# Performance work log

Measured on AMD Instinct MI355X. Metric: run time of the kernel, lower is better.

The kernel has to match this reference:

```python
import jax, jax.numpy as jnp
import numpy as np

H_GRID, W_GRID = 32, 32
KH, KW = 7, 11
NUM_HEADS = 8


def local_window_mask(H, W, kh, kw):
    # Token (h,w) may attend to (h',w') iff |h-h'|<=kh//2 and |w-w'|<=kw//2
    # (equivalent to the padded/cropped construction in the torch module).
    hh = jnp.arange(H)
    ww = jnp.arange(W)
    ok_h = jnp.abs(hh[:, None] - hh[None, :]) <= kh // 2  # [H,H]
    ok_w = jnp.abs(ww[:, None] - ww[None, :]) <= kw // 2  # [W,W]
    ok = ok_h[:, None, :, None] & ok_w[None, :, None, :]  # [H,W,H,W]
    ok = ok.reshape(H * W, H * W)
    return jnp.where(ok, 0.0, -jnp.inf)[None, None]  # [1,1,N,N]


def setup_inputs() -> dict:
    key = jax.random.key(0)
    k1, k2, k3, k4, k5 = jax.random.split(key, 5)
    B, N, E = 8, H_GRID * W_GRID, 256
    return {
        "x": jax.random.normal(k1, (B, N, E), dtype=jnp.float32),
        "qkv_w": jax.random.normal(k2, (3 * E, E), dtype=jnp.float32) * 0.02,
        "qkv_b": jax.random.normal(k3, (3 * E,), dtype=jnp.float32) * 0.02,
        "proj_w": jax.random.normal(k4, (E, E), dtype=jnp.float32) * 0.02,
        "proj_b": jax.random.normal(k5, (E,), dtype=jnp.float32) * 0.02,
    }


def reference(x, qkv_w, qkv_b, proj_w, proj_b):
    B, N, E = x.shape
    dh = E // NUM_HEADS
    scale = E ** (-0.5)  # note: embed_dim scaling, as in the original module
    qkv = x @ qkv_w.T + qkv_b                       # [B,N,3E]
    qkv = qkv.reshape(B, N, 3, NUM_HEADS, dh).transpose(2, 0, 3, 1, 4)
    q, k, v = qkv[0] * scale, qkv[1], qkv[2]        # [B,H,N,dh]
    attn = jnp.einsum('bhnd,bhmd->bhnm', q, k)      # [B,H,N,N]
    attn = attn + local_window_mask(H_GRID, W_GRID, KH, KW)
    attn = jax.nn.softmax(attn, axis=-1)
    out = jnp.einsum('bhnm,bhmd->bhnd', attn, v)    # [B,H,N,dh]
    out = out.transpose(0, 2, 1, 3).reshape(B, N, E)
    return out @ proj_w.T + proj_b
```

## Files before the change

### kernel.cpp

```cpp
#include <hip/hip_runtime.h>
#include <math.h>

constexpr int Bb = 8;
constexpr int Ns = 1024;
constexpr int Es = 256;
constexpr int NH = 8;
constexpr int DH = 32;
constexpr int Mrows = Bb * Ns;
constexpr int NX = Mrows * Es;
constexpr int NQ = 3 * Es * Es;
constexpr int NP = Es * Es;

typedef __bf16 bf16x8 __attribute__((ext_vector_type(8)));
typedef float  f32x4  __attribute__((ext_vector_type(4)));
union U4B8 { uint4 u; bf16x8 b; unsigned short s[8]; };

__device__ __forceinline__ unsigned short f2bf(float f) {
    union { float f; unsigned u; } c; c.f = f;
    unsigned r = (c.u + 0x7FFFu + ((c.u >> 16) & 1u)) >> 16;
    return (unsigned short)r;
}
__device__ __forceinline__ float bf2f(unsigned short h) {
    union { unsigned u; float f; } c; c.u = ((unsigned)h) << 16;
    return c.f;
}

#define GLD 72
#define PST 232

__global__ __launch_bounds__(256)
void cast_all(const float* __restrict__ x, const float* __restrict__ wq,
              const float* __restrict__ wp, unsigned short* __restrict__ xb,
              unsigned short* __restrict__ wqb, unsigned short* __restrict__ wpb)
{
    int i = (blockIdx.x * 256 + threadIdx.x) * 8;
    const float* src; unsigned short* dst;
    if (i < NX)            { src = x  + i;             dst = xb  + i; }
    else if (i < NX + NQ)  { src = wq + (i - NX);      dst = wqb + (i - NX); }
    else                   { src = wp + (i - NX - NQ); dst = wpb + (i - NX - NQ); }
    float4 f0 = *(const float4*)src;
    float4 f1 = *(const float4*)(src + 4);
    U4B8 u;
    u.s[0] = f2bf(f0.x); u.s[1] = f2bf(f0.y); u.s[2] = f2bf(f0.z); u.s[3] = f2bf(f0.w);
    u.s[4] = f2bf(f1.x); u.s[5] = f2bf(f1.y); u.s[6] = f2bf(f1.z); u.s[7] = f2bf(f1.w);
    *(uint4*)dst = u.u;
}

__global__ __launch_bounds__(256, 4)
void qkv_gemm(const unsigned short* __restrict__ A, const unsigned short* __restrict__ W,
              const float* __restrict__ qkv_b,
              unsigned short* __restrict__ qo, unsigned short* __restrict__ ko,
              unsigned short* __restrict__ vto)
{
    __shared__ unsigned short As[64 * GLD];
    __shared__ unsigned short Ws[64 * GLD];

    const int t = threadIdx.x;
    const int m0 = (blockIdx.x & 127) * 64;
    const int j0 = (blockIdx.x >> 7) * 64;

    const int srow = t >> 2;
    const int scol = (t & 3) * 16;

    const int lane = t & 63;
    const int wave = t >> 6;
    const int wm = (wave & 1) * 32;
    const int wn = (wave >> 1) * 32;
    const int fm = lane & 15;
    const int fq = lane >> 4;

    f32x4 acc[2][2];
    #pragma unroll
    for (int i = 0; i < 2; i++)
        #pragma unroll
        for (int j = 0; j < 2; j++)
            acc[i][j] = (f32x4){0.f, 0.f, 0.f, 0.f};

    const unsigned short* Arow = A + (size_t)(m0 + srow) * Es;
    const unsigned short* Wrow = W + (size_t)(j0 + srow) * Es;

    for (int k0 = 0; k0 < Es; k0 += 64) {
        uint4 a0 = *(const uint4*)(Arow + k0 + scol);
        uint4 a1 = *(const uint4*)(Arow + k0 + scol + 8);
        uint4 w0 = *(const uint4*)(Wrow + k0 + scol);
        uint4 w1 = *(const uint4*)(Wrow + k0 + scol + 8);
        __syncthreads();
        *(uint4*)&As[srow * GLD + scol]     = a0;
        *(uint4*)&As[srow * GLD + scol + 8] = a1;
        *(uint4*)&Ws[srow * GLD + scol]     = w0;
        *(uint4*)&Ws[srow * GLD + scol + 8] = w1;
        __syncthreads();
        #pragma unroll
        for (int ks = 0; ks < 64; ks += 32) {
            U4B8 af0, af1, bf0, bf1;
            af0.u = *(const uint4*)&As[(wm +      fm) * GLD + ks + fq * 8];
            af1.u = *(const uint4*)&As[(wm + 16 + fm) * GLD + ks + fq * 8];
            bf0.u = *(const uint4*)&Ws[(wn +      fm) * GLD + ks + fq * 8];
            bf1.u = *(const uint4*)&Ws[(wn + 16 + fm) * GLD + ks + fq * 8];
            acc[0][0] = __builtin_amdgcn_mfma_f32_16x16x32_bf16(af0.b, bf0.b, acc[0][0], 0, 0, 0);
            acc[0][1] = __builtin_amdgcn_mfma_f32_16x16x32_bf16(af0.b, bf1.b, acc[0][1], 0, 0, 0);
            acc[1][0] = __builtin_amdgcn_mfma_f32_16x16x32_bf16(af1.b, bf0.b, acc[1][0], 0, 0, 0);
            acc[1][1] = __builtin_amdgcn_mfma_f32_16x16x32_bf16(af1.b, bf1.b, acc[1][1], 0, 0, 0);
        }
    }

    #pragma unroll
    for (int mt = 0; mt < 2; mt++) {
        #pragma unroll
        for (int nt = 0; nt < 2; nt++) {
            #pragma unroll
            for (int r = 0; r < 4; r++) {
                int row = m0 + wm + mt * 16 + fq * 4 + r;
                int col = j0 + wn + nt * 16 + fm;
                float val = acc[mt][nt][r] + qkv_b[col];
                int part = col >> 8;
                int head = (col >> 5) & 7;
                int d = col & 31;
                int b = row >> 10;
                int n = row & 1023;
                int bh = b * NH + head;
                if (part == 0)
                    qo[((size_t)bh * Ns + n) * DH + d] = f2bf(val * 0.0625f);
                else if (part == 1)
                    ko[((size_t)bh * Ns + n) * DH + d] = f2bf(val);
                else
                    vto[((size_t)bh * DH + d) * Ns + n] = f2bf(val);
            }
        }
    }
}

__global__ __launch_bounds__(256)
void attn_mfma2(const unsigned short* __restrict__ qb, const unsigned short* __restrict__ kb,
                const unsigned short* __restrict__ vtb, unsigned short* __restrict__ aob)
{
    __shared__ unsigned short Pb[32 * PST];
    __shared__ float psum[2][32];

    const int blk = blockIdx.x;
    const int b   = blk & 7;
    const int u   = blk >> 3;
    const int h   = u & 7;
    const int hq  = u >> 3;
    const int bh  = b * NH + h;

    const int t   = threadIdx.x;
    const int lane = t & 63;
    const int w    = t >> 6;
    const int fm = lane & 15;
    const int fq = lane >> 4;

    int n0c = (hq - 3) * 32;
    n0c = n0c < 0 ? 0 : (n0c > Ns - 224 ? Ns - 224 : n0c);

    const int qbase = (w & 1) * 16;
    const int sel   = w >> 1;
    const int dbase = (w >> 1) * 16;

    const unsigned short* vrow = vtb + ((size_t)bh * DH + dbase + fm) * Ns;
    uint4 vpre[7];
    #pragma unroll
    for (int i = 0; i < 7; i++)
        vpre[i] = *(const uint4*)(vrow + n0c + i * 32 + fq * 8);

    U4B8 qa;
    qa.u = *(const uint4*)(qb + ((size_t)bh * Ns + hq * 32 + qbase + fm) * DH + fq * 8);

    f32x4 sv[7];
    #pragma unroll
    for (int i = 0; i < 7; i++) {
        int kt = sel + 2 * i;
        U4B8 kf;
        kf.u = *(const uint4*)(kb + ((size_t)bh * Ns + n0c + kt * 16 + fm) * DH + fq * 8);
        sv[i] = __builtin_amdgcn_mfma_f32_16x16x32_bf16(qa.b, kf.b, (f32x4){0.f,0.f,0.f,0.f}, 0, 0, 0);
    }

    float sm[4] = {0.f, 0.f, 0.f, 0.f};
    #pragma unroll
    for (int i = 0; i < 7; i++) {
        int kt = sel + 2 * i;
        int g = n0c + kt * 16 + fm;
        int gh = g >> 5, gw = g & 31;
        int dhh = gh - hq;
        bool okh = (dhh >= -3) && (dhh <= 3);
        #pragma unroll
        for (int r = 0; r < 4; r++) {
            int qc = qbase + fq * 4 + r;
            int dww = gw - qc;
            bool ok = okh && (dww >= -5) && (dww <= 5);
            float p = ok ? __expf(sv[i][r]) : 0.f;
            unsigned short pu = f2bf(p);
            Pb[qc * PST + kt * 16 + fm] = pu;
            sm[r] += bf2f(pu);
        }
    }
    #pragma unroll
    for (int r = 0; r < 4; r++)
        #pragma unroll
        for (int m = 1; m < 16; m <<= 1)
            sm[r] += __shfl_xor(sm[r], m);
    if (fm == 0) {
        #pragma unroll
        for (int r = 0; r < 4; r++)
            psum[sel][qbase + fq * 4 + r] = sm[r];
    }
    __syncthreads();

    f32x4 acc = (f32x4){0.f, 0.f, 0.f, 0.f};
    #pragma unroll
    for (int i = 0; i < 7; i++) {
        U4B8 pa, vb;
        pa.u = *(const uint4*)&Pb[(qbase + fm) * PST + i * 32 + fq * 8];
        vb.u = vpre[i];
        acc = __builtin_amdgcn_mfma_f32_16x16x32_bf16(pa.b, vb.b, acc, 0, 0, 0);
    }

    #pragma unroll
    for (int r = 0; r < 4; r++) {
        int qq = qbase + fq * 4 + r;
        float inv = 1.f / (psum[0][qq] + psum[1][qq]);
        aob[((size_t)(b * Ns) + hq * 32 + qq) * Es + h * DH + dbase + fm] = f2bf(acc[r] * inv);
    }
}

__global__ __launch_bounds__(256, 4)
void proj_gemm(const unsigned short* __restrict__ A, const unsigned short* __restrict__ Wb,
               const float* __restrict__ bias, float* __restrict__ out)
{
    __shared__ unsigned short As[64 * GLD];
    __shared__ unsigned short Ws[64 * GLD];

    const int t = threadIdx.x;
    const int m0 = (blockIdx.x & 127) * 64;
    const int j0 = (blockIdx.x >> 7) * 64;

    const int srow = t >> 2;
    const int scol = (t & 3) * 16;

    const int lane = t & 63;
    const int wave = t >> 6;
    const int wm = (wave & 1) * 32;
    const int wn = (wave >> 1) * 32;
    const int fm = lane & 15;
    const int fq = lane >> 4;

    f32x4 acc[2][2];
    #pragma unroll
    for (int i = 0; i < 2; i++)
        #pragma unroll
        for (int j = 0; j < 2; j++)
            acc[i][j] = (f32x4){0.f, 0.f, 0.f, 0.f};

    const unsigned short* Arow = A + (size_t)(m0 + srow) * Es;
    const unsigned short* Wrow = Wb + (size_t)(j0 + srow) * Es;

    for (int k0 = 0; k0 < Es; k0 += 64) {
        uint4 a0 = *(const uint4*)(Arow + k0 + scol);
        uint4 a1 = *(const uint4*)(Arow + k0 + scol + 8);
        uint4 w0 = *(const uint4*)(Wrow + k0 + scol);
        uint4 w1 = *(const uint4*)(Wrow + k0 + scol + 8);
        __syncthreads();
        *(uint4*)&As[srow * GLD + scol]     = a0;
        *(uint4*)&As[srow * GLD + scol + 8] = a1;
        *(uint4*)&Ws[srow * GLD + scol]     = w0;
        *(uint4*)&Ws[srow * GLD + scol + 8] = w1;
        __syncthreads();
        #pragma unroll
        for (int ks = 0; ks < 64; ks += 32) {
            U4B8 af0, af1, bf0, bf1;
            af0.u = *(const uint4*)&As[(wm +      fm) * GLD + ks + fq * 8];
            af1.u = *(const uint4*)&As[(wm + 16 + fm) * GLD + ks + fq * 8];
            bf0.u = *(const uint4*)&Ws[(wn +      fm) * GLD + ks + fq * 8];
            bf1.u = *(const uint4*)&Ws[(wn + 16 + fm) * GLD + ks + fq * 8];
            acc[0][0] = __builtin_amdgcn_mfma_f32_16x16x32_bf16(af0.b, bf0.b, acc[0][0], 0, 0, 0);
            acc[0][1] = __builtin_amdgcn_mfma_f32_16x16x32_bf16(af0.b, bf1.b, acc[0][1], 0, 0, 0);
            acc[1][0] = __builtin_amdgcn_mfma_f32_16x16x32_bf16(af1.b, bf0.b, acc[1][0], 0, 0, 0);
            acc[1][1] = __builtin_amdgcn_mfma_f32_16x16x32_bf16(af1.b, bf1.b, acc[1][1], 0, 0, 0);
        }
    }

    #pragma unroll
    for (int mt = 0; mt < 2; mt++) {
        #pragma unroll
        for (int nt = 0; nt < 2; nt++) {
            #pragma unroll
            for (int r = 0; r < 4; r++) {
                int row = m0 + wm + mt * 16 + fq * 4 + r;
                int col = j0 + wn + nt * 16 + fm;
                out[(size_t)row * Es + col] = acc[mt][nt][r] + bias[col];
            }
        }
    }
}

extern "C" void kernel_launch(void* const* d_in, const int* in_sizes, int n_in,
                              void* d_out, int out_size, void* d_ws, size_t ws_size,
                              hipStream_t stream) {
    const float* x      = (const float*)d_in[0];
    const float* qkv_w  = (const float*)d_in[1];
    const float* qkv_b  = (const float*)d_in[2];
    const float* proj_w = (const float*)d_in[3];
    const float* proj_b = (const float*)d_in[4];
    float* out = (float*)d_out;

    unsigned short* xb  = (unsigned short*)d_ws;
    unsigned short* wqb = xb + NX;
    unsigned short* pwb = wqb + NQ;
    unsigned short* qb  = pwb + NP;
    unsigned short* kb  = qb + NX;
    unsigned short* vtb = kb + NX;
    unsigned short* aob = vtb + NX;

    cast_all<<<dim3((NX + NQ + NP) / 8 / 256), dim3(256), 0, stream>>>(
        x, qkv_w, proj_w, xb, wqb, pwb);

    qkv_gemm<<<dim3(1536), dim3(256), 0, stream>>>(xb, wqb, qkv_b, qb, kb, vtb);

    attn_mfma2<<<dim3(Bb * NH * 32), dim3(256), 0, stream>>>(qb, kb, vtb, aob);

    proj_gemm<<<dim3(128 * 4), dim3(256), 0, stream>>>(aob, pwb, proj_b, out);
}
```

Measured before the change: 101.2 us.

## Fuse all four stages into one persistent kernel with grid barriers

```diff
diff --git a/kernel.cpp b/kernel.cpp
--- a/kernel.cpp
+++ b/kernel.cpp
@@ -11,6 +11,13 @@
 constexpr int NQ = 3 * Es * Es;
 constexpr int NP = Es * Es;
 
+constexpr int CAST_UNITS = (NX + NQ + NP) / (8 * 256);
+constexpr int QKV_TILES  = 1536;
+constexpr int ATTN_TILES = Bb * NH * 32;
+constexpr int PROJ_TILES = 512;
+
+constexpr int GRID = 512;
+
 typedef __bf16 bf16x8 __attribute__((ext_vector_type(8)));
 typedef float  f32x4  __attribute__((ext_vector_type(4)));
 union U4B8 { uint4 u; bf16x8 b; unsigned short s[8]; };
@@ -28,266 +35,265 @@
 #define GLD 72
 #define PST 232
 
-__global__ __launch_bounds__(256)
-void cast_all(const float* __restrict__ x, const float* __restrict__ wq,
-              const float* __restrict__ wp, unsigned short* __restrict__ xb,
-              unsigned short* __restrict__ wqb, unsigned short* __restrict__ wpb)
+__device__ __forceinline__ void grid_barrier(unsigned* bar, unsigned nb) {
+    __syncthreads();
+    if (threadIdx.x == 0) {
+        __threadfence();
+        unsigned g = __hip_atomic_load(bar + 1, __ATOMIC_RELAXED, __HIP_MEMORY_SCOPE_AGENT);
+        unsigned a = __hip_atomic_fetch_add(bar, 1u, __ATOMIC_ACQ_REL, __HIP_MEMORY_SCOPE_AGENT);
+        if (a == nb - 1u) {
+            __hip_atomic_store(bar, 0u, __ATOMIC_RELAXED, __HIP_MEMORY_SCOPE_AGENT);
+            __hip_atomic_store(bar + 1, g + 1u, __ATOMIC_RELEASE, __HIP_MEMORY_SCOPE_AGENT);
+        } else {
+            unsigned spins = 0;
+            while (__hip_atomic_load(bar + 1, __ATOMIC_ACQUIRE, __HIP_MEMORY_SCOPE_AGENT) == g) {
+                __builtin_amdgcn_s_sleep(2);
+                if (++spins > (1u << 23)) break;
+            }
+        }
+        __threadfence();
+    }
+    __syncthreads();
+}
+
+__global__ __launch_bounds__(256, 2)
+void mega(const float* __restrict__ x, const float* __restrict__ qkv_w,
+          const float* __restrict__ qkv_b, const float* __restrict__ proj_w,
+          const float* __restrict__ proj_b, float* __restrict__ out,
+          unsigned short* __restrict__ xb, unsigned short* __restrict__ wqb,
+          unsigned short* __restrict__ pwb, unsigned short* __restrict__ qb,
+          unsigned short* __restrict__ kb, unsigned short* __restrict__ vtb,
+          unsigned short* __restrict__ aob, unsigned* bar)
 {
-    int i = (blockIdx.x * 256 + threadIdx.x) * 8;
-    const float* src; unsigned short* dst;
-    if (i < NX)            { src = x  + i;             dst = xb  + i; }
-    else if (i < NX + NQ)  { src = wq + (i - NX);      dst = wqb + (i - NX); }
-    else                   { src = wp + (i - NX - NQ); dst = wpb + (i - NX - NQ); }
-    float4 f0 = *(const float4*)src;
-    float4 f1 = *(const float4*)(src + 4);
-    U4B8 u;
-    u.s[0] = f2bf(f0.x); u.s[1] = f2bf(f0.y); u.s[2] = f2bf(f0.z); u.s[3] = f2bf(f0.w);
-    u.s[4] = f2bf(f1.x); u.s[5] = f2bf(f1.y); u.s[6] = f2bf(f1.z); u.s[7] = f2bf(f1.w);
-    *(uint4*)dst = u.u;
-}
-
-__global__ __launch_bounds__(256, 4)
-void qkv_gemm(const unsigned short* __restrict__ A, const unsigned short* __restrict__ W,
-              const float* __restrict__ qkv_b,
-              unsigned short* __restrict__ qo, unsigned short* __restrict__ ko,
-              unsigned short* __restrict__ vto)
-{
-    __shared__ unsigned short As[64 * GLD];
-    __shared__ unsigned short Ws[64 * GLD];
-
-    const int t = threadIdx.x;
-    const int m0 = (blockIdx.x & 127) * 64;
-    const int j0 = (blockIdx.x >> 7) * 64;
-
+    __shared__ __align__(16) unsigned short SM[2 * 64 * GLD];
+    unsigned short* As = SM;
+    unsigned short* Ws = SM + 64 * GLD;
+    unsigned short* Pb = SM;
+    float (*psum)[32] = (float (*)[32])(SM + 32 * PST);
+
+    const int t    = threadIdx.x;
+    const int lane = t & 63;
+    const int wave = t >> 6;
+    const int fm   = lane & 15;
+    const int fq   = lane >> 4;
     const int srow = t >> 2;
     const int scol = (t & 3) * 16;
-
-    const int lane = t & 63;
-    const int wave = t >> 6;
-    const int wm = (wave & 1) * 32;
-    const int wn = (wave >> 1) * 32;
-    const int fm = lane & 15;
-    const int fq = lane >> 4;
-
-    f32x4 acc[2][2];
-    #pragma unroll
-    for (int i = 0; i < 2; i++)
-        #pragma unroll
-        for (int j = 0; j < 2; j++)
-            acc[i][j] = (f32x4){0.f, 0.f, 0.f, 0.f};
-
-    const unsigned short* Arow = A + (size_t)(m0 + srow) * Es;
-    const unsigned short* Wrow = W + (size_t)(j0 + srow) * Es;
-
-    for (int k0 = 0; k0 < Es; k0 += 64) {
-        uint4 a0 = *(const uint4*)(Arow + k0 + scol);
-        uint4 a1 = *(const uint4*)(Arow + k0 + scol + 8);
-        uint4 w0 = *(const uint4*)(Wrow + k0 + scol);
-        uint4 w1 = *(const uint4*)(Wrow + k0 + scol + 8);
+    const int wm   = (wave & 1) * 32;
+    const int wn   = (wave >> 1) * 32;
+
+    for (int uu = blockIdx.x; uu < CAST_UNITS; uu += GRID) {
+        int i = (uu * 256 + t) * 8;
+        const float* src; unsigned short* dst;
+        if (i < NX)            { src = x      + i;             dst = xb  + i; }
+        else if (i < NX + NQ)  { src = qkv_w  + (i - NX);      dst = wqb + (i - NX); }
+        else                   { src = proj_w + (i - NX - NQ); dst = pwb + (i - NX - NQ); }
+        float4 f0 = *(const float4*)src;
+        float4 f1 = *(const float4*)(src + 4);
+        U4B8 uo;
+        uo.s[0] = f2bf(f0.x); uo.s[1] = f2bf(f0.y); uo.s[2] = f2bf(f0.z); uo.s[3] = f2bf(f0.w);
+        uo.s[4] = f2bf(f1.x); uo.s[5] = f2bf(f1.y); uo.s[6] = f2bf(f1.z); uo.s[7] = f2bf(f1.w);
+        *(uint4*)dst = uo.u;
+    }
+    grid_barrier(bar, GRID);
+
+    for (int tile = blockIdx.x; tile < QKV_TILES; tile += GRID) {
+        const int m0 = (tile & 127) * 64;
+        const int j0 = (tile >> 7) * 64;
+
+        f32x4 acc[2][2];
+        #pragma unroll
+        for (int i = 0; i < 2; i++)
+            #pragma unroll
+            for (int j = 0; j < 2; j++)
+                acc[i][j] = (f32x4){0.f, 0.f, 0.f, 0.f};
+
+        const unsigned short* Arow = xb  + (size_t)(m0 + srow) * Es;
+        const unsigned short* Wrow = wqb + (size_t)(j0 + srow) * Es;
+
+        for (int k0 = 0; k0 < Es; k0 += 64) {
+            uint4 a0 = *(const uint4*)(Arow + k0 + scol);
+            uint4 a1 = *(const uint4*)(Arow + k0 + scol + 8);
+            uint4 w0 = *(const uint4*)(Wrow + k0 + scol);
+            uint4 w1 = *(const uint4*)(Wrow + k0 + scol + 8);
+            __syncthreads();
+            *(uint4*)&As[srow * GLD + scol]     = a0;
+            *(uint4*)&As[srow * GLD + scol + 8] = a1;
+            *(uint4*)&Ws[srow * GLD + scol]     = w0;
+            *(uint4*)&Ws[srow * GLD + scol + 8] = w1;
+            __syncthreads();
+            #pragma unroll
+            for (int ks = 0; ks < 64; ks += 32) {
+                U4B8 af0, af1, bf0, bf1;
+                af0.u = *(const uint4*)&As[(wm +      fm) * GLD + ks + fq * 8];
+                af1.u = *(const uint4*)&As[(wm + 16 + fm) * GLD + ks + fq * 8];
+                bf0.u = *(const uint4*)&Ws[(wn +      fm) * GLD + ks + fq * 8];
+                bf1.u = *(const uint4*)&Ws[(wn + 16 + fm) * GLD + ks + fq * 8];
+                acc[0][0] = __builtin_amdgcn_mfma_f32_16x16x32_bf16(af0.b, bf0.b, acc[0][0], 0, 0, 0);
+                acc[0][1] = __builtin_amdgcn_mfma_f32_16x16x32_bf16(af0.b, bf1.b, acc[0][1], 0, 0, 0);
+                acc[1][0] = __builtin_amdgcn_mfma_f32_16x16x32_bf16(af1.b, bf0.b, acc[1][0], 0, 0, 0);
+                acc[1][1] = __builtin_amdgcn_mfma_f32_16x16x32_bf16(af1.b, bf1.b, acc[1][1], 0, 0, 0);
+            }
+        }
+
+        #pragma unroll
+        for (int mt = 0; mt < 2; mt++) {
+            #pragma unroll
+            for (int nt = 0; nt < 2; nt++) {
+                #pragma unroll
+                for (int r = 0; r < 4; r++) {
+                    int row = m0 + wm + mt * 16 + fq * 4 + r;
+                    int col = j0 + wn + nt * 16 + fm;
+                    float val = acc[mt][nt][r] + qkv_b[col];
+                    int part = col >> 8;
+                    int head = (col >> 5) & 7;
+                    int d = col & 31;
+                    int b = row >> 10;
+                    int n = row & 1023;
+                    int bh = b * NH + head;
+                    if (part == 0)
+                        qb[((size_t)bh * Ns + n) * DH + d] = f2bf(val * 0.0625f);
+                    else if (part == 1)
+                        kb[((size_t)bh * Ns + n) * DH + d] = f2bf(val);
+                    else
+                        vtb[((size_t)bh * DH + d) * Ns + n] = f2bf(val);
+                }
+            }
+        }
+    }
+    grid_barrier(bar, GRID);
+
+    for (int blk = blockIdx.x; blk < ATTN_TILES; blk += GRID) {
+        const int b  = blk & 7;
+        const int u2 = blk >> 3;
+        const int h  = u2 & 7;
+        const int hq = u2 >> 3;
+        const int bh = b * NH + h;
+
         __syncthreads();
-        *(uint4*)&As[srow * GLD + scol]     = a0;
-        *(uint4*)&As[srow * GLD + scol + 8] = a1;
-        *(uint4*)&Ws[srow * GLD + scol]     = w0;
-        *(uint4*)&Ws[srow * GLD + scol + 8] = w1;
+
+        int n0c = (hq - 3) * 32;
+        n0c = n0c < 0 ? 0 : (n0c > Ns - 224 ? Ns - 224 : n0c);
+
+        const int qbase = (wave & 1) * 16;
+        const int sel   = wave >> 1;
+        const int dbase = (wave >> 1) * 16;
+
+        const unsigned short* vrow = vtb + ((size_t)bh * DH + dbase + fm) * Ns;
+        uint4 vpre[7];
+        #pragma unroll
+        for (int i = 0; i < 7; i++)
+            vpre[i] = *(const uint4*)(vrow + n0c + i * 32 + fq * 8);
+
+        U4B8 qa;
+        qa.u = *(const uint4*)(qb + ((size_t)bh * Ns + hq * 32 + qbase + fm) * DH + fq * 8);
+
+        f32x4 sv[7];
+        #pragma unroll
+        for (int i = 0; i < 7; i++) {
+            int kt = sel + 2 * i;
+            U4B8 kf;
+            kf.u = *(const uint4*)(kb + ((size_t)bh * Ns + n0c + kt * 16 + fm) * DH + fq * 8);
+            sv[i] = __builtin_amdgcn_mfma_f32_16x16x32_bf16(qa.b, kf.b, (f32x4){0.f,0.f,0.f,0.f}, 0, 0, 0);
+        }
+
+        float sm[4] = {0.f, 0.f, 0.f, 0.f};
+        #pragma unroll
+        for (int i = 0; i < 7; i++) {
+            int kt = sel + 2 * i;
+            int g = n0c + kt * 16 + fm;
+            int gh = g >> 5, gw = g & 31;
+            int dhh = gh - hq;
+            bool okh = (dhh >= -3) && (dhh <= 3);
+            #pragma unroll
+            for (int r = 0; r < 4; r++) {
+                int qc = qbase + fq * 4 + r;
+                int dww = gw - qc;
+                bool ok = okh && (dww >= -5) && (dww <= 5);
+                float p = ok ? __expf(sv[i][r]) : 0.f;
+                unsigned short pu = f2bf(p);
+                Pb[qc * PST + kt * 16 + fm] = pu;
+                sm[r] += bf2f(pu);
+            }
+        }
+        #pragma unroll
+        for (int r = 0; r < 4; r++)
+            #pragma unroll
+            for (int m = 1; m < 16; m <<= 1)
+                sm[r] += __shfl_xor(sm[r], m);
+        if (fm == 0) {
+            #pragma unroll
+            for (int r = 0; r < 4; r++)
+                psum[sel][qbase + fq * 4 + r] = sm[r];
+        }
         __syncthreads();
-        #pragma unroll
-        for (int ks = 0; ks < 64; ks += 32) {
-            U4B8 af0, af1, bf0, bf1;
-            af0.u = *(const uint4*)&As[(wm +      fm) * GLD + ks + fq * 8];
-            af1.u = *(const uint4*)&As[(wm + 16 + fm) * GLD + ks + fq * 8];
-            bf0.u = *(const uint4*)&Ws[(wn +      fm) * GLD + ks + fq * 8];
-            bf1.u = *(const uint4*)&Ws[(wn + 16 + fm) * GLD + ks + fq * 8];
-            acc[0][0] = __builtin_amdgcn_mfma_f32_16x16x32_bf16(af0.b, bf0.b, acc[0][0], 0, 0, 0);
-            acc[0][1] = __builtin_amdgcn_mfma_f32_16x16x32_bf16(af0.b, bf1.b, acc[0][1], 0, 0, 0);
-            acc[1][0] = __builtin_amdgcn_mfma_f32_16x16x32_bf16(af1.b, bf0.b, acc[1][0], 0, 0, 0);
-            acc[1][1] = __builtin_amdgcn_mfma_f32_16x16x32_bf16(af1.b, bf1.b, acc[1][1], 0, 0, 0);
-        }
-    }
-
-    #pragma unroll
-    for (int mt = 0; mt < 2; mt++) {
-        #pragma unroll
-        for (int nt = 0; nt < 2; nt++) {
-            #pragma unroll
-            for (int r = 0; r < 4; r++) {
-                int row = m0 + wm + mt * 16 + fq * 4 + r;
-                int col = j0 + wn + nt * 16 + fm;
-                float val = acc[mt][nt][r] + qkv_b[col];
-                int part = col >> 8;
-                int head = (col >> 5) & 7;
-                int d = col & 31;
-                int b = row >> 10;
-                int n = row & 1023;
-                int bh = b * NH + head;
-                if (part == 0)
-                    qo[((size_t)bh * Ns + n) * DH + d] = f2bf(val * 0.0625f);
-                else if (part == 1)
-                    ko[((size_t)bh * Ns + n) * DH + d] = f2bf(val);
-                else
-                    vto[((size_t)bh * DH + d) * Ns + n] = f2bf(val);
-            }
-        }
-    }
-}
-
-__global__ __launch_bounds__(256)
-void attn_mfma2(const unsigned short* __restrict__ qb, const unsigned short* __restrict__ kb,
-                const unsigned short* __restrict__ vtb, unsigned short* __restrict__ aob)
-{
-    __shared__ unsigned short Pb[32 * PST];
-    __shared__ float psum[2][32];
-
-    const int blk = blockIdx.x;
-    const int b   = blk & 7;
-    const int u   = blk >> 3;
-    const int h   = u & 7;
-    const int hq  = u >> 3;
-    const int bh  = b * NH + h;
-
-    const int t   = threadIdx.x;
-    const int lane = t & 63;
-    const int w    = t >> 6;
-    const int fm = lane & 15;
-    const int fq = lane >> 4;
-
-    int n0c = (hq - 3) * 32;
-    n0c = n0c < 0 ? 0 : (n0c > Ns - 224 ? Ns - 224 : n0c);
-
-    const int qbase = (w & 1) * 16;
-    const int sel   = w >> 1;
-    const int dbase = (w >> 1) * 16;
-
-    const unsigned short* vrow = vtb + ((size_t)bh * DH + dbase + fm) * Ns;
-    uint4 vpre[7];
-    #pragma unroll
-    for (int i = 0; i < 7; i++)
-        vpre[i] = *(const uint4*)(vrow + n0c + i * 32 + fq * 8);
-
-    U4B8 qa;
-    qa.u = *(const uint4*)(qb + ((size_t)bh * Ns + hq * 32 + qbase + fm) * DH + fq * 8);
-
-    f32x4 sv[7];
-    #pragma unroll
-    for (int i = 0; i < 7; i++) {
-        int kt = sel + 2 * i;
-        U4B8 kf;
-        kf.u = *(const uint4*)(kb + ((size_t)bh * Ns + n0c + kt * 16 + fm) * DH + fq * 8);
-        sv[i] = __builtin_amdgcn_mfma_f32_16x16x32_bf16(qa.b, kf.b, (f32x4){0.f,0.f,0.f,0.f}, 0, 0, 0);
-    }
-
-    float sm[4] = {0.f, 0.f, 0.f, 0.f};
-    #pragma unroll
-    for (int i = 0; i < 7; i++) {
-        int kt = sel + 2 * i;
-        int g = n0c + kt * 16 + fm;
-        int gh = g >> 5, gw = g & 31;
-        int dhh = gh - hq;
-        bool okh = (dhh >= -3) && (dhh <= 3);
+
+        f32x4 acc = (f32x4){0.f, 0.f, 0.f, 0.f};
+        #pragma unroll
+        for (int i = 0; i < 7; i++) {
+            U4B8 pa, vb;
+            pa.u = *(const uint4*)&Pb[(qbase + fm) * PST + i * 32 + fq * 8];
+            vb.u = vpre[i];
+            acc = __builtin_amdgcn_mfma_f32_16x16x32_bf16(pa.b, vb.b, acc, 0, 0, 0);
+        }
+
         #pragma unroll
         for (int r = 0; r < 4; r++) {
-            int qc = qbase + fq * 4 + r;
-            int dww = gw - qc;
-            bool ok = okh && (dww >= -5) && (dww <= 5);
-            float p = ok ? __expf(sv[i][r]) : 0.f;
-            unsigned short pu = f2bf(p);
-            Pb[qc * PST + kt * 16 + fm] = pu;
-            sm[r] += bf2f(pu);
-        }
-    }
-    #pragma unroll
-    for (int r = 0; r < 4; r++)
-        #pragma unroll
-        for (int m = 1; m < 16; m <<= 1)
-            sm[r] += __shfl_xor(sm[r], m);
-    if (fm == 0) {
-        #pragma unroll
-        for (int r = 0; r < 4; r++)
-            psum[sel][qbase + fq * 4 + r] = sm[r];
-    }
-    __syncthreads();
-
-    f32x4 acc = (f32x4){0.f, 0.f, 0.f, 0.f};
-    #pragma unroll
-    for (int i = 0; i < 7; i++) {
-        U4B8 pa, vb;
-        pa.u = *(const uint4*)&Pb[(qbase + fm) * PST + i * 32 + fq * 8];
-        vb.u = vpre[i];
-        acc = __builtin_amdgcn_mfma_f32_16x16x32_bf16(pa.b, vb.b, acc, 0, 0, 0);
-    }
-
-    #pragma unroll
-    for (int r = 0; r < 4; r++) {
-        int qq = qbase + fq * 4 + r;
-        float inv = 1.f / (psum[0][qq] + psum[1][qq]);
-        aob[((size_t)(b * Ns) + hq * 32 + qq) * Es + h * DH + dbase + fm] = f2bf(acc[r] * inv);
-    }
-}
-
-__global__ __launch_bounds__(256, 4)
-void proj_gemm(const unsigned short* __restrict__ A, const unsigned short* __restrict__ Wb,
-               const float* __restrict__ bias, float* __restrict__ out)
-{
-    __shared__ unsigned short As[64 * GLD];
-    __shared__ unsigned short Ws[64 * GLD];
-
-    const int t = threadIdx.x;
-    const int m0 = (blockIdx.x & 127) * 64;
-    const int j0 = (blockIdx.x >> 7) * 64;
-
-    const int srow = t >> 2;
-    const int scol = (t & 3) * 16;
-
-    const int lane = t & 63;
-    const int wave = t >> 6;
-    const int wm = (wave & 1) * 32;
-    const int wn = (wave >> 1) * 32;
-    const int fm = lane & 15;
-    const int fq = lane >> 4;
-
-    f32x4 acc[2][2];
-    #pragma unroll
-    for (int i = 0; i < 2; i++)
-        #pragma unroll
-        for (int j = 0; j < 2; j++)
-            acc[i][j] = (f32x4){0.f, 0.f, 0.f, 0.f};
-
-    const unsigned short* Arow = A + (size_t)(m0 + srow) * Es;
-    const unsigned short* Wrow = Wb + (size_t)(j0 + srow) * Es;
-
-    for (int k0 = 0; k0 < Es; k0 += 64) {
-        uint4 a0 = *(const uint4*)(Arow + k0 + scol);
-        uint4 a1 = *(const uint4*)(Arow + k0 + scol + 8);
-        uint4 w0 = *(const uint4*)(Wrow + k0 + scol);
-        uint4 w1 = *(const uint4*)(Wrow + k0 + scol + 8);
-        __syncthreads();
-        *(uint4*)&As[srow * GLD + scol]     = a0;
-        *(uint4*)&As[srow * GLD + scol + 8] = a1;
-        *(uint4*)&Ws[srow * GLD + scol]     = w0;
-        *(uint4*)&Ws[srow * GLD + scol + 8] = w1;
-        __syncthreads();
-        #pragma unroll
-        for (int ks = 0; ks < 64; ks += 32) {
-            U4B8 af0, af1, bf0, bf1;
-            af0.u = *(const uint4*)&As[(wm +      fm) * GLD + ks + fq * 8];
-            af1.u = *(const uint4*)&As[(wm + 16 + fm) * GLD + ks + fq * 8];
-            bf0.u = *(const uint4*)&Ws[(wn +      fm) * GLD + ks + fq * 8];
-            bf1.u = *(const uint4*)&Ws[(wn + 16 + fm) * GLD + ks + fq * 8];
-            acc[0][0] = __builtin_amdgcn_mfma_f32_16x16x32_bf16(af0.b, bf0.b, acc[0][0], 0, 0, 0);
-            acc[0][1] = __builtin_amdgcn_mfma_f32_16x16x32_bf16(af0.b, bf1.b, acc[0][1], 0, 0, 0);
-            acc[1][0] = __builtin_amdgcn_mfma_f32_16x16x32_bf16(af1.b, bf0.b, acc[1][0], 0, 0, 0);
-            acc[1][1] = __builtin_amdgcn_mfma_f32_16x16x32_bf16(af1.b, bf1.b, acc[1][1], 0, 0, 0);
-        }
-    }
-
-    #pragma unroll
-    for (int mt = 0; mt < 2; mt++) {
-        #pragma unroll
-        for (int nt = 0; nt < 2; nt++) {
-            #pragma unroll
-            for (int r = 0; r < 4; r++) {
-                int row = m0 + wm + mt * 16 + fq * 4 + r;
-                int col = j0 + wn + nt * 16 + fm;
-                out[(size_t)row * Es + col] = acc[mt][nt][r] + bias[col];
+            int qq = qbase + fq * 4 + r;
+            float inv = 1.f / (psum[0][qq] + psum[1][qq]);
+            aob[((size_t)(b * Ns) + hq * 32 + qq) * Es + h * DH + dbase + fm] = f2bf(acc[r] * inv);
+        }
+    }
+    grid_barrier(bar, GRID);
+
+    for (int tile = blockIdx.x; tile < PROJ_TILES; tile += GRID) {
+        const int m0 = (tile & 127) * 64;
+        const int j0 = (tile >> 7) * 64;
+
+        f32x4 acc[2][2];
+        #pragma unroll
+        for (int i = 0; i < 2; i++)
+            #pragma unroll
+            for (int j = 0; j < 2; j++)
+                acc[i][j] = (f32x4){0.f, 0.f, 0.f, 0.f};
+
+        const unsigned short* Arow = aob + (size_t)(m0 + srow) * Es;
+        const unsigned short* Wrow = pwb + (size_t)(j0 + srow) * Es;
+
+        for (int k0 = 0; k0 < Es; k0 += 64) {
+            uint4 a0 = *(const uint4*)(Arow + k0 + scol);
+            uint4 a1 = *(const uint4*)(Arow + k0 + scol + 8);
+            uint4 w0 = *(const uint4*)(Wrow + k0 + scol);
+            uint4 w1 = *(const uint4*)(Wrow + k0 + scol + 8);
+            __syncthreads();
+            *(uint4*)&As[srow * GLD + scol]     = a0;
+            *(uint4*)&As[srow * GLD + scol + 8] = a1;
+            *(uint4*)&Ws[srow * GLD + scol]     = w0;
+            *(uint4*)&Ws[srow * GLD + scol + 8] = w1;
+            __syncthreads();
+            #pragma unroll
+            for (int ks = 0; ks < 64; ks += 32) {
+                U4B8 af0, af1, bf0, bf1;
+                af0.u = *(const uint4*)&As[(wm +      fm) * GLD + ks + fq * 8];
+                af1.u = *(const uint4*)&As[(wm + 16 + fm) * GLD + ks + fq * 8];
+                bf0.u = *(const uint4*)&Ws[(wn +      fm) * GLD + ks + fq * 8];
+                bf1.u = *(const uint4*)&Ws[(wn + 16 + fm) * GLD + ks + fq * 8];
+                acc[0][0] = __builtin_amdgcn_mfma_f32_16x16x32_bf16(af0.b, bf0.b, acc[0][0], 0, 0, 0);
+                acc[0][1] = __builtin_amdgcn_mfma_f32_16x16x32_bf16(af0.b, bf1.b, acc[0][1], 0, 0, 0);
+                acc[1][0] = __builtin_amdgcn_mfma_f32_16x16x32_bf16(af1.b, bf0.b, acc[1][0], 0, 0, 0);
+                acc[1][1] = __builtin_amdgcn_mfma_f32_16x16x32_bf16(af1.b, bf1.b, acc[1][1], 0, 0, 0);
+            }
+        }
+
+        #pragma unroll
+        for (int mt = 0; mt < 2; mt++) {
+            #pragma unroll
+            for (int nt = 0; nt < 2; nt++) {
+                #pragma unroll
+                for (int r = 0; r < 4; r++) {
+                    int row = m0 + wm + mt * 16 + fq * 4 + r;
+                    int col = j0 + wn + nt * 16 + fm;
+                    out[(size_t)row * Es + col] = acc[mt][nt][r] + proj_b[col];
+                }
             }
         }
     }
@@ -310,13 +316,11 @@
     unsigned short* kb  = qb + NX;
     unsigned short* vtb = kb + NX;
     unsigned short* aob = vtb + NX;
-
-    cast_all<<<dim3((NX + NQ + NP) / 8 / 256), dim3(256), 0, stream>>>(
-        x, qkv_w, proj_w, xb, wqb, pwb);
-
-    qkv_gemm<<<dim3(1536), dim3(256), 0, stream>>>(xb, wqb, qkv_b, qb, kb, vtb);
-
-    attn_mfma2<<<dim3(Bb * NH * 32), dim3(256), 0, stream>>>(qb, kb, vtb, aob);
-
-    proj_gemm<<<dim3(128 * 4), dim3(256), 0, stream>>>(aob, pwb, proj_b, out);
-}
+    unsigned* bar = (unsigned*)(aob + NX + 64);
+
+    hipMemsetAsync(bar, 0, 8, stream);
+
+    mega<<<dim3(GRID), dim3(256), 0, stream>>>(
+        x, qkv_w, qkv_b, proj_w, proj_b, out,
+        xb, wqb, pwb, qb, kb, vtb, aob, bar);
+}
```

Result: slower. 338.2 us (+234.2%).
